# Optimization experiments

Measured on AMD Instinct MI355X. Metric: run time of the kernel, lower is better.

Reference implementation:

```python
import jax, jax.numpy as jnp
import numpy as np

B, T, S0, S1 = 128, 16384, 64, 64  # batch, num_tiles, sizes[0], sizes[1]


def setup_inputs() -> dict:
    key = jax.random.key(0)
    k0, k1, k2, k3, k4 = jax.random.split(key, 5)
    x = jax.random.normal(k0, (B, 1, S0), dtype=jnp.float32)
    # Conv1d(1, T*S1, kernel_size=S0) weights, squeezed over the in-channel dim.
    fan1 = 1.0 / np.sqrt(S0)
    W1 = jax.random.uniform(k1, (T * S1, S0), jnp.float32, -fan1, fan1)
    b1 = jax.random.uniform(k2, (T * S1,), jnp.float32, -fan1, fan1)
    # Conv1d(T, T, kernel_size=S1, groups=T): one (1, S1) filter per tile.
    fan2 = 1.0 / np.sqrt(S1)
    W2 = jax.random.uniform(k3, (T, S1), jnp.float32, -fan2, fan2)
    b2 = jax.random.uniform(k4, (T,), jnp.float32, -fan2, fan2)
    return {"x": x, "W1": W1, "b1": b1, "W2": W2, "b2": b2}


def reference(x, W1, b1, W2, b2):
    # Conv1d(1, T*S1, kernel=S0) on length-S0 input == GEMM -> length-1 output.
    h = jnp.einsum("bs,cs->bc", x[:, 0, :], W1) + b1        # (B, T*S1)
    h = jax.nn.relu(h).reshape(x.shape[0], T, S1)            # (B, T, S1)
    # Grouped Conv1d (groups=T, 1 ch/group, kernel=S1) == per-tile dot product.
    y = jnp.einsum("btk,tk->bt", h, W2) + b2                 # (B, T)
    return (2.0 * y)[:, :, None]                             # (B, T, 1)
```

## Files before the change

### kernel.cpp

```cpp
#include <hip/hip_runtime.h>
#include <hip/hip_bf16.h>

namespace {

constexpr int T_DIM = 16384;
constexpr int NT    = 16;
constexpr int NCHUNK = 1024;

typedef __attribute__((ext_vector_type(8))) short bf16x8;
typedef __attribute__((ext_vector_type(4))) float f32x4;

__device__ inline short f2bf(float f) {
    union { __hip_bfloat16 h; short s; } u;
    u.h = __float2bfloat16(f);
    return u.s;
}

}

__global__ __launch_bounds__(256, 4) void fgbn_kernel(
    const float* __restrict__ x,
    const float* __restrict__ W1,
    const float* __restrict__ b1,
    const float* __restrict__ W2,
    const float* __restrict__ b2,
    float* __restrict__ out)
{
    __shared__ float lds[2][NCHUNK * 4];

    const int tid  = threadIdx.x;
    const int lane = tid & 63;
    const int wave = tid >> 6;
    const int l15  = lane & 15;
    const int l4   = lane >> 4;

    bf16x8 afrag[2][2];
    #pragma unroll
    for (int rf = 0; rf < 2; ++rf) {
        const int row = wave * 32 + rf * 16 + l15;
        #pragma unroll
        for (int ks = 0; ks < 2; ++ks) {
            const float* src = x + row * 64 + ks * 32 + l4 * 8;
            f32x4 v0 = *reinterpret_cast<const f32x4*>(src);
            f32x4 v1 = *reinterpret_cast<const f32x4*>(src + 4);
            bf16x8 r;
            r[0] = f2bf(v0[0]); r[1] = f2bf(v0[1]); r[2] = f2bf(v0[2]); r[3] = f2bf(v0[3]);
            r[4] = f2bf(v1[0]); r[5] = f2bf(v1[1]); r[6] = f2bf(v1[2]); r[7] = f2bf(v1[3]);
            afrag[rf][ks] = r;
        }
    }

    const int t0 = blockIdx.x * NT;

    auto stage = [&](int buf, int t) {
        const char* w1t = (const char*)W1 + (size_t)t * 16384;
        #pragma unroll
        for (int it = 0; it < 4; ++it) {
            const int c = wave * 256 + it * 64 + lane;
            const int g = c ^ ((c >> 4) & 7);
            __builtin_amdgcn_global_load_lds(
                (const __attribute__((address_space(1))) unsigned int*)(w1t + (size_t)g * 16),
                (__attribute__((address_space(3))) unsigned int*)&lds[buf][c * 4],
                16, 0, 0);
        }
    };

    float b1v[4], w2v[4];
    #pragma unroll
    for (int nf = 0; nf < 4; ++nf) {
        b1v[nf] = b1[t0 * 64 + nf * 16 + l15];
        w2v[nf] = W2[t0 * 64 + nf * 16 + l15];
    }
    float b2v = b2[t0];

    stage(0, t0);
    __syncthreads();

    f32x4 outv[2] = {{0.f,0.f,0.f,0.f},{0.f,0.f,0.f,0.f}};

    for (int ti = 0; ti < NT; ++ti) {
        const int t = t0 + ti;

        float b1n[4], w2n[4], b2n = 0.f;
        if (ti + 1 < NT) {
            stage((ti + 1) & 1, t + 1);
            #pragma unroll
            for (int nf = 0; nf < 4; ++nf) {
                b1n[nf] = b1[(t + 1) * 64 + nf * 16 + l15];
                w2n[nf] = W2[(t + 1) * 64 + nf * 16 + l15];
            }
            b2n = b2[t + 1];
        }

        const float* lbuf = lds[ti & 1];
        f32x4 acc[2][4];
        #pragma unroll
        for (int rf = 0; rf < 2; ++rf)
            #pragma unroll
            for (int nf = 0; nf < 4; ++nf)
                acc[rf][nf] = (f32x4){0.f, 0.f, 0.f, 0.f};

        #pragma unroll
        for (int nf = 0; nf < 4; ++nf) {
            const int j = nf * 16 + l15;
            const int sw = j & 7;
            bf16x8 bks[2];
            #pragma unroll
            for (int ks = 0; ks < 2; ++ks) {
                const int c0 = j * 16 + ks * 8 + l4 * 2;
                f32x4 v0 = *reinterpret_cast<const f32x4*>(&lbuf[(c0 ^ sw) * 4]);
                f32x4 v1 = *reinterpret_cast<const f32x4*>(&lbuf[((c0 + 1) ^ sw) * 4]);
                bf16x8 r;
                r[0] = f2bf(v0[0]); r[1] = f2bf(v0[1]); r[2] = f2bf(v0[2]); r[3] = f2bf(v0[3]);
                r[4] = f2bf(v1[0]); r[5] = f2bf(v1[1]); r[6] = f2bf(v1[2]); r[7] = f2bf(v1[3]);
                bks[ks] = r;
            }
            #pragma unroll
            for (int ks = 0; ks < 2; ++ks)
                #pragma unroll
                for (int rf = 0; rf < 2; ++rf)
                    acc[rf][nf] = __builtin_amdgcn_mfma_f32_16x16x32_bf16(
                        afrag[rf][ks], bks[ks], acc[rf][nf], 0, 0, 0);
        }

        #pragma unroll
        for (int rf = 0; rf < 2; ++rf) {
            #pragma unroll
            for (int r = 0; r < 4; ++r) {
                float s = 0.f;
                #pragma unroll
                for (int nf = 0; nf < 4; ++nf) {
                    float p = fmaxf(acc[rf][nf][r] + b1v[nf], 0.f);
                    s = fmaf(p, w2v[nf], s);
                }
                s += __shfl_xor(s, 1);
                s += __shfl_xor(s, 2);
                s += __shfl_xor(s, 4);
                s += __shfl_xor(s, 8);
                const float v = 2.f * (s + b2v);
                outv[rf][r] = (l15 == ti) ? v : outv[rf][r];
            }
        }

        if (ti + 1 < NT) {
            #pragma unroll
            for (int nf = 0; nf < 4; ++nf) { b1v[nf] = b1n[nf]; w2v[nf] = w2n[nf]; }
            b2v = b2n;
        }
        __syncthreads();
    }

    #pragma unroll
    for (int rf = 0; rf < 2; ++rf)
        #pragma unroll
        for (int r = 0; r < 4; ++r) {
            const int brow = wave * 32 + rf * 16 + l4 * 4 + r;
            out[(size_t)brow * T_DIM + t0 + l15] = outv[rf][r];
        }
}

extern "C" void kernel_launch(void* const* d_in, const int* in_sizes, int n_in,
                              void* d_out, int out_size, void* d_ws, size_t ws_size,
                              hipStream_t stream) {
    const float* x  = (const float*)d_in[0];
    const float* W1 = (const float*)d_in[1];
    const float* b1 = (const float*)d_in[2];
    const float* W2 = (const float*)d_in[3];
    const float* b2 = (const float*)d_in[4];
    float* out = (float*)d_out;

    dim3 grid(T_DIM / NT);
    dim3 block(256);
    hipLaunchKernelGGL(fgbn_kernel, grid, block, 0, stream,
                       x, W1, b1, W2, b2, out);
}
```

Before: 58.31 us.

## Deepen W1 prefetch to four LDS buffers with explicit vmcnt waits

Replaces the double-buffered W1 staging with a four-slot ring that prefetches two tiles ahead, gated by explicit s_waitcnt vmcnt counts and a single barrier per iteration. The per-tile b1 and W2 vectors are loaded once into LDS with async global-to-LDS copies, and b2 is read once per lane. The goal is to keep more HBM traffic in flight on this bandwidth-bound W1 stream and to cut per-iteration register shuffling and one barrier. In exchange, LDS use per block rises to roughly 72KB and launch bounds drop to 2 blocks per CU, which lowers occupancy.

New measurement: 68.85 us. +18.1%, slower.

```diff
diff --git a/kernel.cpp b/kernel.cpp
--- a/kernel.cpp
+++ b/kernel.cpp
@@ -5,7 +5,7 @@
 
 constexpr int T_DIM = 16384;
 constexpr int NT    = 16;
-constexpr int NCHUNK = 1024;
+constexpr int NBUF  = 4;
 
 typedef __attribute__((ext_vector_type(8))) short bf16x8;
 typedef __attribute__((ext_vector_type(4))) float f32x4;
@@ -18,7 +18,7 @@
 
 }
 
-__global__ __launch_bounds__(256, 4) void fgbn_kernel(
+__global__ __launch_bounds__(256, 2) void fgbn_kernel(
     const float* __restrict__ x,
     const float* __restrict__ W1,
     const float* __restrict__ b1,
@@ -26,13 +26,16 @@
     const float* __restrict__ b2,
     float* __restrict__ out)
 {
-    __shared__ float lds[2][NCHUNK * 4];
+    __shared__ float tile[NBUF][4096];
+    __shared__ float b1s[NT * 64];
+    __shared__ float w2s[NT * 64];
 
     const int tid  = threadIdx.x;
     const int lane = tid & 63;
     const int wave = tid >> 6;
     const int l15  = lane & 15;
     const int l4   = lane >> 4;
+    const int t0   = blockIdx.x * NT;
 
     bf16x8 afrag[2][2];
     #pragma unroll
@@ -49,8 +52,14 @@
             afrag[rf][ks] = r;
         }
     }
+    const float b2lane = b2[t0 + l15];
 
-    const int t0 = blockIdx.x * NT;
+    __builtin_amdgcn_global_load_lds(
+        (const __attribute__((address_space(1))) unsigned int*)(b1 + t0 * 64 + tid * 4),
+        (__attribute__((address_space(3))) unsigned int*)&b1s[tid * 4], 16, 0, 0);
+    __builtin_amdgcn_global_load_lds(
+        (const __attribute__((address_space(1))) unsigned int*)(W2 + t0 * 64 + tid * 4),
+        (__attribute__((address_space(3))) unsigned int*)&w2s[tid * 4], 16, 0, 0);
 
     auto stage = [&](int buf, int t) {
         const char* w1t = (const char*)W1 + (size_t)t * 16384;
@@ -60,39 +69,33 @@
             const int g = c ^ ((c >> 4) & 7);
             __builtin_amdgcn_global_load_lds(
                 (const __attribute__((address_space(1))) unsigned int*)(w1t + (size_t)g * 16),
-                (__attribute__((address_space(3))) unsigned int*)&lds[buf][c * 4],
+                (__attribute__((address_space(3))) unsigned int*)&tile[buf][c * 4],
                 16, 0, 0);
         }
     };
 
-    float b1v[4], w2v[4];
-    #pragma unroll
-    for (int nf = 0; nf < 4; ++nf) {
-        b1v[nf] = b1[t0 * 64 + nf * 16 + l15];
-        w2v[nf] = W2[t0 * 64 + nf * 16 + l15];
-    }
-    float b2v = b2[t0];
-
     stage(0, t0);
-    __syncthreads();
+    stage(1, t0 + 1);
 
     f32x4 outv[2] = {{0.f,0.f,0.f,0.f},{0.f,0.f,0.f,0.f}};
 
     for (int ti = 0; ti < NT; ++ti) {
-        const int t = t0 + ti;
+        if (ti + 2 < NT) stage((ti + 2) & (NBUF - 1), t0 + ti + 2);
 
-        float b1n[4], w2n[4], b2n = 0.f;
-        if (ti + 1 < NT) {
-            stage((ti + 1) & 1, t + 1);
-            #pragma unroll
-            for (int nf = 0; nf < 4; ++nf) {
-                b1n[nf] = b1[(t + 1) * 64 + nf * 16 + l15];
-                w2n[nf] = W2[(t + 1) * 64 + nf * 16 + l15];
-            }
-            b2n = b2[t + 1];
+        if (ti < NT - 2)       asm volatile("s_waitcnt vmcnt(8)" ::: "memory");
+        else if (ti == NT - 2) asm volatile("s_waitcnt vmcnt(4)" ::: "memory");
+        else                   asm volatile("s_waitcnt vmcnt(0)" ::: "memory");
+        __builtin_amdgcn_s_barrier();
+
+        const float* lbuf = tile[ti & (NBUF - 1)];
+
+        float b1v[4], w2v[4];
+        #pragma unroll
+        for (int nf = 0; nf < 4; ++nf) {
+            b1v[nf] = b1s[ti * 64 + nf * 16 + l15];
+            w2v[nf] = w2s[ti * 64 + nf * 16 + l15];
         }
 
-        const float* lbuf = lds[ti & 1];
         f32x4 acc[2][4];
         #pragma unroll
         for (int rf = 0; rf < 2; ++rf)
@@ -137,17 +140,10 @@
                 s += __shfl_xor(s, 2);
                 s += __shfl_xor(s, 4);
                 s += __shfl_xor(s, 8);
-                const float v = 2.f * (s + b2v);
+                const float v = 2.f * (s + b2lane);
                 outv[rf][r] = (l15 == ti) ? v : outv[rf][r];
             }
         }
-
-        if (ti + 1 < NT) {
-            #pragma unroll
-            for (int nf = 0; nf < 4; ++nf) { b1v[nf] = b1n[nf]; w2v[nf] = w2n[nf]; }
-            b2v = b2n;
-        }
-        __syncthreads();
     }
 
     #pragma unroll
```
